# Performance work log

Measured on AMD Instinct MI355X. Metric: run time of the kernel, lower is better.

The kernel has to match this reference:

```python
import jax, jax.numpy as jnp
import numpy as np

B, S, D, H, F = 64, 256, 512, 8, 2048
NB = 2
L = NB + 2 * NB  # blocks_1 (NB) + blocks_2 (2*NB) = 6 attention layers
DH = D // H
FC1, FC2 = 512, 256  # final_fc_dim, final_fc_dim // 2


def setup_inputs() -> dict:
    key = jax.random.key(0)
    ks = jax.random.split(key, 32)
    w = lambda k, shape, s: jax.random.normal(k, shape, dtype=jnp.float32) * s
    sD = D ** -0.5
    return {
        "q_embed_data": w(ks[0], (B, S, D), 1.0),
        "qa_embed_data": w(ks[1], (B, S, D), 1.0),
        "Wq": w(ks[2], (L, D, D), sD), "bq": jnp.zeros((L, D), jnp.float32),
        "Wk": w(ks[3], (L, D, D), sD), "bk": jnp.zeros((L, D), jnp.float32),
        "Wv": w(ks[4], (L, D, D), sD), "bv": jnp.zeros((L, D), jnp.float32),
        "Wo": w(ks[5], (L, D, D), sD), "bo": jnp.zeros((L, D), jnp.float32),
        "gammas": w(ks[6], (L, H), 1.0),
        "ln1_g": jnp.ones((L, D), jnp.float32), "ln1_b": jnp.zeros((L, D), jnp.float32),
        "W1": w(ks[7], (L, D, F), sD), "b1": jnp.zeros((L, F), jnp.float32),
        "W2": w(ks[8], (L, F, D), F ** -0.5), "b2": jnp.zeros((L, D), jnp.float32),
        "ln2_g": jnp.ones((L, D), jnp.float32), "ln2_b": jnp.zeros((L, D), jnp.float32),
        "O1": w(ks[9], (2 * D, FC1), (2 * D) ** -0.5), "bO1": jnp.zeros((FC1,), jnp.float32),
        "O2": w(ks[10], (FC1, FC2), FC1 ** -0.5), "bO2": jnp.zeros((FC2,), jnp.float32),
        "O3": w(ks[11], (FC2, 1), FC2 ** -0.5), "bO3": jnp.zeros((1,), jnp.float32),
    }


def _layer_norm(x, g, b):
    mu = x.mean(-1, keepdims=True)
    var = ((x - mu) ** 2).mean(-1, keepdims=True)
    return (x - mu) * jax.lax.rsqrt(var + 1e-5) * g + b


def _akt_attention(q, k, v, mask, gamma, zero_pad):
    # q,k,v: [B,H,S,DH]; mask: [S,S] bool; gamma: [H]
    neg = jnp.float32(-1e32)
    scores = jnp.einsum('bhqd,bhkd->bhqk', q, k) / np.sqrt(DH).astype(np.float32)
    # monotonic distance-decay (detached in the original): softmax'd scores -> cumulative distance
    sm = jax.nn.softmax(jnp.where(mask, scores, neg), axis=-1) * mask
    sm = jax.lax.stop_gradient(sm)
    distcum = jnp.cumsum(sm, axis=-1)
    disttot = jnp.sum(sm, axis=-1, keepdims=True)
    idx = jnp.arange(S)
    pos = jnp.abs(idx[:, None] - idx[None, :]).astype(jnp.float32)  # |x1 - x2|
    dist = jnp.sqrt(jnp.clip((disttot - distcum) * pos, 0.0, None))
    g = -jax.nn.softplus(gamma)[None, :, None, None]
    total_effect = jnp.clip(jnp.exp(dist * g), 1e-5, 1e5)
    scores = jnp.where(mask, scores * total_effect, neg)
    attn = jax.nn.softmax(scores, axis=-1)
    if zero_pad:
        attn = attn.at[:, :, 0, :].set(0.0)  # zero first query row
    out = jnp.einsum('bhqk,bhkd->bhqd', attn, v)
    return out, attn


def reference(q_embed_data, qa_embed_data, Wq, bq, Wk, bk, Wv, bv, Wo, bo, gammas,
              ln1_g, ln1_b, W1, b1, W2, b2, ln2_g, ln2_b, O1, bO1, O2, bO2, O3, bO3):
    idx = jnp.arange(S)
    mask_incl = idx[:, None] >= idx[None, :]  # mask==1: current + past
    mask_excl = idx[:, None] > idx[None, :]   # mask==0: strictly past

    def block(i, query, key_, vals, incl, zero_pad, apply_pos):
        proj = lambda x, W, b: (x @ W + b).reshape(B, S, H, DH).transpose(0, 2, 1, 3)
        qh, kh, vh = proj(query, Wq[i], bq[i]), proj(key_, Wk[i], bk[i]), proj(vals, Wv[i], bv[i])
        o, attn = _akt_attention(qh, kh, vh, mask_incl if incl else mask_excl, gammas[i], zero_pad)
        o = o.transpose(0, 2, 1, 3).reshape(B, S, D) @ Wo[i] + bo[i]
        q2 = _layer_norm(query + o, ln1_g[i], ln1_b[i])
        if apply_pos:
            h = jax.nn.relu(q2 @ W1[i] + b1[i]) @ W2[i] + b2[i]
            q2 = _layer_norm(q2 + h, ln2_g[i], ln2_b[i])
        return q2, attn

    y = qa_embed_data
    x = q_embed_data
    li = 0
    for _ in range(NB):  # blocks_1: knowledge encoder, self-attn, mask=1
        y, _ = block(li, y, y, y, incl=True, zero_pad=False, apply_pos=True)
        li += 1
    attn = None
    flag_first = True
    for _ in range(2 * NB):  # blocks_2: alternating question self-attn / knowledge retriever
        if flag_first:
            x, _ = block(li, x, x, x, incl=True, zero_pad=False, apply_pos=False)
            flag_first = False
        else:
            x, attn = block(li, x, x, y, incl=False, zero_pad=True, apply_pos=True)
            flag_first = True
        li += 1

    concat_q = jnp.concatenate([x, q_embed_data], axis=-1)  # [B,S,2D]
    h = jax.nn.relu(concat_q @ O1 + bO1)
    h = jax.nn.relu(h @ O2 + bO2)
    preds = jax.nn.sigmoid((h @ O3 + bO3)[..., 0])  # [B,S]
    return preds
```

## Files before the change

kernel.cpp:

```cpp
#include <hip/hip_runtime.h>

typedef unsigned short u16;
typedef unsigned int u32;
typedef short short8 __attribute__((ext_vector_type(8)));
typedef float f32x4 __attribute__((ext_vector_type(4)));

#define DEV static __device__ __forceinline__

DEV u16 f2bf(float f) {
  u32 u = __builtin_bit_cast(u32, f);
  u32 r = u + 0x7FFFu + ((u >> 16) & 1u);
  return (u16)(r >> 16);
}
DEV float bf2f(u16 h) { u32 u = ((u32)h) << 16; return __builtin_bit_cast(float, u); }

DEV u32 cvtpk(float lo, float hi_) {
  u32 r;
  asm("v_cvt_pk_bf16_f32 %0, %1, %2" : "=v"(r) : "v"(lo), "v"(hi_));
  return r;
}

DEV void async16(const u16* g, u16* l) {
  __builtin_amdgcn_global_load_lds((const __attribute__((address_space(1))) void*)g,
                                   (__attribute__((address_space(3))) void*)l, 16, 0, 0);
}

template<bool RELU, bool OUTBF, bool RESID, bool SPLIT3>
__global__ __launch_bounds__(256, 2) void gemm_kernel(
    const u16* __restrict__ A, const u16* __restrict__ A2, int KA,
    int lda, int lda2,
    const u16* __restrict__ Bt, int K,
    const float* __restrict__ bias, const float* __restrict__ resid,
    float* __restrict__ Cf, u16* __restrict__ Cb, u16* __restrict__ Cb2, u16* __restrict__ Cb3,
    int ldc)
{
  __shared__ u16 smem[2][16384];
  const int tid = threadIdx.x, wave = tid >> 6, lane = tid & 63;
  const int m0 = blockIdx.x * 128, n0 = blockIdx.y * 128;
  const int wr = wave >> 1, wc = wave & 1;
  const int lj = lane & 15, hi = lane >> 4;

  f32x4 acc[4][4];
  const f32x4 zz = {0.f, 0.f, 0.f, 0.f};
#pragma unroll
  for (int i = 0; i < 4; i++)
#pragma unroll
    for (int j = 0; j < 4; j++) acc[i][j] = zz;

  const int nkt = K / 64;

  auto stage = [&](int buf, int kt) {
    int kofs = kt * 64;
    const u16* sa; int la;
    if (kofs < KA) { sa = A + kofs; la = lda; }
    else           { sa = A2 + (kofs - KA); la = lda2; }
#pragma unroll
    for (int i = 0; i < 8; i++) {
      int c = wave * 8 + i;
      if (c < 16) {
        const u16* g = sa + (size_t)(m0 + c * 8 + (lane >> 3)) * la + (lane & 7) * 8;
        async16(g, &smem[buf][c * 512]);
      } else {
        const u16* g = Bt + (size_t)(n0 + (c - 16) * 8 + (lane >> 3)) * K + kofs + (lane & 7) * 8;
        async16(g, &smem[buf][c * 512]);
      }
    }
  };

  stage(0, 0);
  int cur = 0;
  for (int kt = 0; kt < nkt; kt++) {
    __syncthreads();
    if (kt + 1 < nkt) stage(cur ^ 1, kt + 1);
    const u16* la_ = &smem[cur][0];
    const u16* lb_ = &smem[cur][8192];
#pragma unroll
    for (int ks = 0; ks < 2; ks++) {
      short8 af[4], bfr[4];
#pragma unroll
      for (int mi = 0; mi < 4; mi++)
        af[mi] = *(const short8*)(la_ + (wr * 64 + mi * 16 + lj) * 64 + ks * 32 + hi * 8);
#pragma unroll
      for (int ni = 0; ni < 4; ni++)
        bfr[ni] = *(const short8*)(lb_ + (wc * 64 + ni * 16 + lj) * 64 + ks * 32 + hi * 8);
#pragma unroll
      for (int mi = 0; mi < 4; mi++)
#pragma unroll
        for (int ni = 0; ni < 4; ni++)
          acc[mi][ni] = __builtin_amdgcn_mfma_f32_16x16x32_bf16(af[mi], bfr[ni], acc[mi][ni], 0, 0, 0);
    }
    cur ^= 1;
  }

  u16* outB = Cb;
  int nloc = n0;
  if (SPLIT3) {
    int sec = n0 >> 9;
    outB = (sec == 0) ? Cb : (sec == 1) ? Cb2 : Cb3;
    nloc = n0 & 511;
  }

  float bv[4];
#pragma unroll
  for (int ni = 0; ni < 4; ni++) bv[ni] = bias[n0 + wc * 64 + ni * 16 + lj];
#pragma unroll
  for (int mi = 0; mi < 4; mi++)
#pragma unroll
    for (int r = 0; r < 4; r++) {
      int row = m0 + wr * 64 + mi * 16 + hi * 4 + r;
      size_t rb = (size_t)row * ldc;
#pragma unroll
      for (int ni = 0; ni < 4; ni++) {
        int col = nloc + wc * 64 + ni * 16 + lj;
        float v = acc[mi][ni][r] + bv[ni];
        if (RESID) v += resid[rb + col];
        if (RELU) v = fmaxf(v, 0.f);
        if (OUTBF) outB[rb + col] = f2bf(v);
        else Cf[rb + col] = v;
      }
    }
}

template<bool INCL, bool ZP>
__global__ __launch_bounds__(512) void attn_kernel(
    const u16* __restrict__ qb, const u16* __restrict__ kb, const u16* __restrict__ vb,
    u16* __restrict__ ob, const float* __restrict__ gammas, int li)
{
  __shared__ u16 smem[32768];
  const int tid = threadIdx.x, wave = tid >> 6, lane = tid & 63;
  const int h = blockIdx.x, b = blockIdx.y;
  const int lj = lane & 15, hi = lane >> 4;
  const size_t rowbase = (size_t)b * 256 * 512 + h * 64;

#pragma unroll
  for (int p = 0; p < 2; p++) {
    int r2 = p * 128 + (tid >> 3) * 2;
    int cc = (tid & 7) * 8;
    union { uint4 v; u16 e[8]; } v0, v1;
    uint4 k0 = *(const uint4*)(kb + rowbase + (size_t)r2 * 512 + cc);
    uint4 k1 = *(const uint4*)(kb + rowbase + (size_t)(r2 + 1) * 512 + cc);
    v0.v = *(const uint4*)(vb + rowbase + (size_t)r2 * 512 + cc);
    v1.v = *(const uint4*)(vb + rowbase + (size_t)(r2 + 1) * 512 + cc);
    *(uint4*)((char*)smem + r2 * 128 + ((cc * 2) ^ ((r2 & 7) << 4))) = k0;
    *(uint4*)((char*)smem + (r2 + 1) * 128 + ((cc * 2) ^ (((r2 + 1) & 7) << 4))) = k1;
#pragma unroll
    for (int i = 0; i < 8; i++) {
      int d = cc + i;
      u32 pk = (u32)v0.e[i] | ((u32)v1.e[i] << 16);
      *(u32*)((char*)smem + 32768 + d * 512 + ((2 * r2) ^ ((d & 7) << 4))) = pk;
    }
  }

  const int qbase = wave * 32;
  const int nrf = 2 * wave + 2;
  const int nsp = wave + 1;

  short8 qfa[2][2];
#pragma unroll
  for (int cf = 0; cf < 2; cf++)
#pragma unroll
    for (int s = 0; s < 2; s++)
      qfa[cf][s] = *(const short8*)(qb + rowbase + (size_t)(qbase + cf * 16 + lj) * 512 + s * 32 + hi * 8);

  float gm = gammas[li * 8 + h];
  float geff = -(gm > 20.f ? gm : log1pf(__expf(gm)));

  __syncthreads();

  const f32x4 zz = {0.f, 0.f, 0.f, 0.f};
  const int hsel = hi >> 1;
  const int sbase = lj + 32 * (hi & 1);

#pragma unroll
  for (int cf = 0; cf < 2; cf++) {
    const int q = qbase + cf * 16 + lj;

    f32x4 acc[16];
#pragma unroll
    for (int rf = 0; rf < 16; rf++) acc[rf] = zz;

#pragma unroll
    for (int rf = 0; rf < 16; rf++) {
      if (rf >= nrf) continue;
      int row = rf * 16 + lj;
#pragma unroll
      for (int s = 0; s < 2; s++) {
        short8 kf = *(const short8*)((char*)smem + row * 128 + ((s * 64 + hi * 16) ^ ((row & 7) << 4)));
        acc[rf] = __builtin_amdgcn_mfma_f32_16x16x32_bf16(kf, qfa[cf][s], acc[rf], 0, 0, 0);
      }
    }

    float mx = -1e30f;
#pragma unroll
    for (int rf = 0; rf < 16; rf++) {
      if (rf >= nrf) continue;
#pragma unroll
      for (int r = 0; r < 4; r++) {
        acc[rf][r] *= 0.125f;
        int k = rf * 16 + hi * 4 + r;
        bool valid = INCL ? (k <= q) : (k < q);
        mx = fmaxf(mx, valid ? acc[rf][r] : -1e30f);
      }
    }
    mx = fmaxf(mx, __shfl_xor(mx, 16));
    mx = fmaxf(mx, __shfl_xor(mx, 32));
    float sum = 0.f;
#pragma unroll
    for (int rf = 0; rf < 16; rf++) {
      if (rf >= nrf) continue;
#pragma unroll
      for (int r = 0; r < 4; r++) {
        int k = rf * 16 + hi * 4 + r;
        bool valid = INCL ? (k <= q) : (k < q);
        sum += valid ? __expf(acc[rf][r] - mx) : 0.f;
      }
    }
    sum += __shfl_xor(sum, 16);
    sum += __shfl_xor(sum, 32);
    float m1 = mx;
    float inv1 = sum > 0.f ? 1.f / sum : 0.f;
    float dtot = sum > 0.f ? 1.f : 0.f;

    float run = 0.f;
#pragma unroll
    for (int rf = 0; rf < 16; rf++) {
      if (rf >= nrf) continue;
      float p[4];
      float pa = 0.f;
#pragma unroll
      for (int r = 0; r < 4; r++) {
        int k = rf * 16 + hi * 4 + r;
        bool valid = INCL ? (k <= q) : (k < q);
        float smv = valid ? __expf(acc[rf][r] - m1) * inv1 : 0.f;
        pa += smv;
        p[r] = pa;
      }
      float t = p[3];
      float v = t;
      float u1 = __shfl_up(v, 16); v += (hi >= 1) ? u1 : 0.f;
      float u2 = __shfl_up(v, 32); v += (hi >= 2) ? u2 : 0.f;
      float T = __shfl(v, lj + 48);
      float cbase = run + (v - t);
#pragma unroll
      for (int r = 0; r < 4; r++) {
        int k = rf * 16 + hi * 4 + r;
        bool valid = INCL ? (k <= q) : (k < q);
        float tail = fmaxf(dtot - (cbase + p[r]), 0.f);
        float pos = (float)(q - k);
        float dist = sqrtf(tail * pos);
        float te = fmaxf(__expf(dist * geff), 1e-5f);
        acc[rf][r] = valid ? acc[rf][r] * te : -1e32f;
      }
      run += T;
    }

    float mx2 = -3.0e38f;
#pragma unroll
    for (int rf = 0; rf < 16; rf++) {
      if (rf >= nrf) continue;
#pragma unroll
      for (int r = 0; r < 4; r++) mx2 = fmaxf(mx2, acc[rf][r]);
    }
    mx2 = fmaxf(mx2, __shfl_xor(mx2, 16));
    mx2 = fmaxf(mx2, __shfl_xor(mx2, 32));
    float sum2 = 0.f;
#pragma unroll
    for (int rf = 0; rf < 16; rf++) {
      if (rf >= nrf) continue;
#pragma unroll
      for (int r = 0; r < 4; r++) {
        float ev = __expf(acc[rf][r] - mx2);
        acc[rf][r] = ev;
        sum2 += ev;
      }
    }
    sum2 += __shfl_xor(sum2, 16);
    sum2 += __shfl_xor(sum2, 32);
    float inv = 1.f / sum2;
    if (ZP) { if (q == 0) inv = 0.f; }
#pragma unroll
    for (int rf = 0; rf < 16; rf++) {
      if (rf >= nrf) continue;
#pragma unroll
      for (int r = 0; r < 4; r++) acc[rf][r] *= inv;
    }

    f32x4 oacc[4];
#pragma unroll
    for (int j = 0; j < 4; j++) oacc[j] = zz;

#pragma unroll
    for (int sp = 0; sp < 8; sp++) {
      if (sp >= nsp) continue;
      u32 a0 = cvtpk(acc[2 * sp][0],     acc[2 * sp][1]);
      u32 a1 = cvtpk(acc[2 * sp][2],     acc[2 * sp][3]);
      u32 b0 = cvtpk(acc[2 * sp + 1][0], acc[2 * sp + 1][1]);
      u32 b1 = cvtpk(acc[2 * sp + 1][2], acc[2 * sp + 1][3]);
      u32 pw[4];
#pragma unroll
      for (int t = 0; t < 4; t++) {
        int src = sbase + 16 * (t >> 1);
        u32 za = (u32)__shfl((int)((t & 1) ? a1 : a0), src);
        u32 zb = (u32)__shfl((int)((t & 1) ? b1 : b0), src);
        pw[t] = hsel ? zb : za;
      }
      short8 pf = __builtin_bit_cast(short8, *(uint4*)pw);
#pragma unroll
      for (int nf = 0; nf < 4; nf++) {
        int d = nf * 16 + lj;
        short8 vf = *(const short8*)((char*)smem + 32768 + d * 512 + ((sp * 64 + hi * 16) ^ ((d & 7) << 4)));
        oacc[nf] = __builtin_amdgcn_mfma_f32_16x16x32_bf16(pf, vf, oacc[nf], 0, 0, 0);
      }
    }

#pragma unroll
    for (int r = 0; r < 4; r++) {
      int qr = qbase + cf * 16 + hi * 4 + r;
      size_t obase = (size_t)(b * 256 + qr) * 512 + h * 64;
#pragma unroll
      for (int nf = 0; nf < 4; nf++)
        ob[obase + nf * 16 + lj] = f2bf(oacc[nf][r]);
    }
  }
}

__global__ __launch_bounds__(256) void ln_kernel(const float* __restrict__ x,
    const float* __restrict__ g, const float* __restrict__ bt,
    float* __restrict__ outF, u16* __restrict__ outB)
{
  int row = blockIdx.x * 4 + (threadIdx.x >> 6), lane = threadIdx.x & 63;
  const float* xr = x + (size_t)row * 512 + lane * 8;
  float4 a = *(const float4*)xr;
  float4 c = *(const float4*)(xr + 4);
  float s = a.x + a.y + a.z + a.w + c.x + c.y + c.z + c.w;
  float q = a.x*a.x + a.y*a.y + a.z*a.z + a.w*a.w + c.x*c.x + c.y*c.y + c.z*c.z + c.w*c.w;
#pragma unroll
  for (int m = 1; m <= 32; m <<= 1) { s += __shfl_xor(s, m); q += __shfl_xor(q, m); }
  float mu = s * (1.f / 512.f);
  float var = q * (1.f / 512.f) - mu * mu;
  float rs = rsqrtf(fmaxf(var, 0.f) + 1e-5f);
  const float* gr = g + lane * 8; const float* br = bt + lane * 8;
  float4 g0 = *(const float4*)gr, g1v = *(const float4*)(gr + 4);
  float4 b0 = *(const float4*)br, b1v = *(const float4*)(br + 4);
  float y[8];
  y[0]=(a.x-mu)*rs*g0.x+b0.x; y[1]=(a.y-mu)*rs*g0.y+b0.y; y[2]=(a.z-mu)*rs*g0.z+b0.z; y[3]=(a.w-mu)*rs*g0.w+b0.w;
  y[4]=(c.x-mu)*rs*g1v.x+b1v.x; y[5]=(c.y-mu)*rs*g1v.y+b1v.y; y[6]=(c.z-mu)*rs*g1v.z+b1v.z; y[7]=(c.w-mu)*rs*g1v.w+b1v.w;
  float* of = outF + (size_t)row * 512 + lane * 8;
  *(float4*)of = make_float4(y[0], y[1], y[2], y[3]);
  *(float4*)(of + 4) = make_float4(y[4], y[5], y[6], y[7]);
  union { uint4 v; u16 e[8]; } pk;
#pragma unroll
  for (int i = 0; i < 8; i++) pk.e[i] = f2bf(y[i]);
  *(uint4*)(outB + (size_t)row * 512 + lane * 8) = pk.v;
}

__global__ void cvt_kernel(const float* __restrict__ in, u16* __restrict__ out, int n8)
{
  int i = blockIdx.x * 256 + threadIdx.x;
  if (i >= n8) return;
  float4 a = ((const float4*)in)[2 * i], c = ((const float4*)in)[2 * i + 1];
  union { uint4 v; u16 e[8]; } pk;
  pk.e[0]=f2bf(a.x); pk.e[1]=f2bf(a.y); pk.e[2]=f2bf(a.z); pk.e[3]=f2bf(a.w);
  pk.e[4]=f2bf(c.x); pk.e[5]=f2bf(c.y); pk.e[6]=f2bf(c.z); pk.e[7]=f2bf(c.w);
  ((uint4*)out)[i] = pk.v;
}

__global__ void trans_kernel(const float* __restrict__ in, u16* __restrict__ out,
                             int R, int C, size_t istr, size_t ostr)
{
  __shared__ float tile[32][33];
  in += (size_t)blockIdx.z * istr;
  out += (size_t)blockIdx.z * ostr;
  int c0 = blockIdx.x * 32, r0 = blockIdx.y * 32;
  int tx = threadIdx.x & 31, ty = threadIdx.x >> 5;
#pragma unroll
  for (int i = 0; i < 4; i++) tile[ty + i * 8][tx] = in[(size_t)(r0 + ty + i * 8) * C + c0 + tx];
  __syncthreads();
#pragma unroll
  for (int i = 0; i < 4; i++) out[(size_t)(c0 + ty + i * 8) * R + r0 + tx] = f2bf(tile[tx][ty + i * 8]);
}

__global__ void bias_concat_kernel(const float* __restrict__ bq, const float* __restrict__ bk,
                                   const float* __restrict__ bv, float* __restrict__ out)
{
  int t = blockIdx.x * 256 + threadIdx.x;
  if (t >= 6 * 1536) return;
  int li = t / 1536, c = t % 1536;
  float v = (c < 512) ? bq[li * 512 + c]
          : (c < 1024) ? bk[li * 512 + c - 512]
                       : bv[li * 512 + c - 1024];
  out[t] = v;
}

__global__ __launch_bounds__(256) void pred_kernel(const u16* __restrict__ h2,
    const float* __restrict__ O3, const float* __restrict__ bO3, float* __restrict__ out)
{
  int row = blockIdx.x * 4 + (threadIdx.x >> 6), lane = threadIdx.x & 63;
  union { uint2 v; u16 e[4]; } hv;
  hv.v = *(const uint2*)(h2 + (size_t)row * 256 + lane * 4);
  float d = 0.f;
#pragma unroll
  for (int i = 0; i < 4; i++) d += bf2f(hv.e[i]) * O3[lane * 4 + i];
#pragma unroll
  for (int m = 1; m <= 32; m <<= 1) d += __shfl_xor(d, m);
  if (lane == 0) out[row] = 1.f / (1.f + expf(-(d + bO3[0])));
}

extern "C" void kernel_launch(void* const* d_in, const int* in_sizes, int n_in,
                              void* d_out, int out_size, void* d_ws, size_t ws_size,
                              hipStream_t stream)
{
  const float* qe   = (const float*)d_in[0];
  const float* qa   = (const float*)d_in[1];
  const float* Wq   = (const float*)d_in[2];  const float* bq  = (const float*)d_in[3];
  const float* Wk   = (const float*)d_in[4];  const float* bk  = (const float*)d_in[5];
  const float* Wv   = (const float*)d_in[6];  const float* bv  = (const float*)d_in[7];
  const float* Wo   = (const float*)d_in[8];  const float* bo  = (const float*)d_in[9];
  const float* gam  = (const float*)d_in[10];
  const float* ln1g = (const float*)d_in[11]; const float* ln1b = (const float*)d_in[12];
  const float* W1   = (const float*)d_in[13]; const float* b1  = (const float*)d_in[14];
  const float* W2   = (const float*)d_in[15]; const float* b2  = (const float*)d_in[16];
  const float* ln2g = (const float*)d_in[17]; const float* ln2b = (const float*)d_in[18];
  const float* O1   = (const float*)d_in[19]; const float* bO1 = (const float*)d_in[20];
  const float* O2   = (const float*)d_in[21]; const float* bO2 = (const float*)d_in[22];
  const float* O3   = (const float*)d_in[23]; const float* bO3 = (const float*)d_in[24];
  float* preds = (float*)d_out;

  const int M = 16384;
  const int BIG = 0x3fffffff;
  char* ws = (char*)d_ws;
  size_t off = 0;
  auto alloc = [&](size_t bytes) { char* p = ws + off; off += (bytes + 255) & ~(size_t)255; return p; };

  u16* wqkvt = (u16*)alloc((size_t)6*1536*512*2);
  u16* wot   = (u16*)alloc((size_t)6*512*512*2);
  u16* w1t   = (u16*)alloc((size_t)6*2048*512*2);
  u16* w2t   = (u16*)alloc((size_t)6*512*2048*2);
  u16* o1t   = (u16*)alloc((size_t)512*1024*2);
  u16* o2t   = (u16*)alloc((size_t)256*512*2);
  float* bqkv = (float*)alloc((size_t)6*1536*4);
  u16* qx  = (u16*)alloc((size_t)M*512*2);
  u16* sA  = (u16*)alloc((size_t)M*512*2);
  u16* sB  = (u16*)alloc((size_t)M*512*2);
  float* g1 = (float*)alloc((size_t)M*512*4);
  u16* region = (u16*)alloc((size_t)M*2048*2);
  u16* qbf = region;
  u16* kbf = region + (size_t)M*512;
  u16* vbf = region + (size_t)2*M*512;
  u16* obf = region + (size_t)3*M*512;
  u16* h1  = region;
  u16* hd1 = region;
  u16* hd2 = region + (size_t)2*M*512;
  (void)ws_size; (void)in_sizes; (void)n_in; (void)out_size;

  trans_kernel<<<dim3(16, 16, 6), 256, 0, stream>>>(Wq, wqkvt,                          512, 512,  (size_t)512*512,  (size_t)1536*512);
  trans_kernel<<<dim3(16, 16, 6), 256, 0, stream>>>(Wk, wqkvt + (size_t)512*512,        512, 512,  (size_t)512*512,  (size_t)1536*512);
  trans_kernel<<<dim3(16, 16, 6), 256, 0, stream>>>(Wv, wqkvt + (size_t)1024*512,       512, 512,  (size_t)512*512,  (size_t)1536*512);
  trans_kernel<<<dim3(16, 16, 6), 256, 0, stream>>>(Wo, wot,                            512, 512,  (size_t)512*512,  (size_t)512*512);
  trans_kernel<<<dim3(64, 16, 6), 256, 0, stream>>>(W1, w1t,                            512, 2048, (size_t)512*2048, (size_t)2048*512);
  trans_kernel<<<dim3(16, 64, 6), 256, 0, stream>>>(W2, w2t,                            2048, 512, (size_t)2048*512, (size_t)512*2048);
  trans_kernel<<<dim3(16, 32, 1), 256, 0, stream>>>(O1, o1t,                            1024, 512, 0, 0);
  trans_kernel<<<dim3(8, 16, 1),  256, 0, stream>>>(O2, o2t,                            512, 256,  0, 0);
  bias_concat_kernel<<<36, 256, 0, stream>>>(bq, bk, bv, bqkv);
  cvt_kernel<<<4096, 256, 0, stream>>>(qe, qx, M * 512 / 8);
  cvt_kernel<<<4096, 256, 0, stream>>>(qa, sA, M * 512 / 8);

  const u16* curB = sA;
  const float* curF = qa;
  const u16* yfin = nullptr;
  const dim3 gP(128, 4), gF1(128, 16), gA(8, 64);

  for (int li = 0; li < 6; li++) {
    bool ffn  = (li == 0 || li == 1 || li == 3 || li == 5);
    bool excl = (li == 3 || li == 5);
    size_t wqkv_off = (size_t)li * 1536 * 512;

    if (!excl) {
      gemm_kernel<false, true, false, true><<<dim3(128, 12), 256, 0, stream>>>(
          curB, curB, BIG, 512, 512, wqkvt + wqkv_off, 512, bqkv + li * 1536,
          nullptr, nullptr, qbf, kbf, vbf, 512);
    } else {
      gemm_kernel<false, true, false, true><<<dim3(128, 8), 256, 0, stream>>>(
          curB, curB, BIG, 512, 512, wqkvt + wqkv_off, 512, bqkv + li * 1536,
          nullptr, nullptr, qbf, kbf, nullptr, 512);
      gemm_kernel<false, true, false, false><<<dim3(128, 4), 256, 0, stream>>>(
          yfin, yfin, BIG, 512, 512, wqkvt + wqkv_off + (size_t)1024 * 512, 512, bv + li * 512,
          nullptr, nullptr, vbf, nullptr, nullptr, 512);
    }

    if (!excl) attn_kernel<true,  false><<<gA, 512, 0, stream>>>(qbf, kbf, vbf, obf, gam, li);
    else       attn_kernel<false, true ><<<gA, 512, 0, stream>>>(qbf, kbf, vbf, obf, gam, li);

    gemm_kernel<false, false, true, false><<<gP, 256, 0, stream>>>(
        obf, obf, BIG, 512, 512, wot + (size_t)li * 512 * 512, 512, bo + li * 512,
        curF, g1, nullptr, nullptr, nullptr, 512);

    ln_kernel<<<4096, 256, 0, stream>>>(g1, ln1g + li * 512, ln1b + li * 512, g1, sB);
    curB = sB; curF = g1;

    if (ffn) {
      gemm_kernel<true, true, false, false><<<gF1, 256, 0, stream>>>(
          curB, curB, BIG, 512, 512, w1t + (size_t)li * 2048 * 512, 512, b1 + li * 2048,
          nullptr, nullptr, h1, nullptr, nullptr, 2048);
      gemm_kernel<false, false, true, false><<<gP, 256, 0, stream>>>(
          h1, h1, BIG, 2048, 2048, w2t + (size_t)li * 512 * 2048, 2048, b2 + li * 512,
          g1, g1, nullptr, nullptr, nullptr, 512);
      u16* nB = (li < 2) ? sA : sB;
      ln_kernel<<<4096, 256, 0, stream>>>(g1, ln2g + li * 512, ln2b + li * 512, g1, nB);
      curB = nB;
    }
    if (li == 1) { yfin = curB; curB = qx; curF = qe; }
  }

  gemm_kernel<true, true, false, false><<<dim3(128, 4), 256, 0, stream>>>(
      curB, qx, 512, 512, 512, o1t, 1024, bO1, nullptr, nullptr, hd1, nullptr, nullptr, 512);
  gemm_kernel<true, true, false, false><<<dim3(128, 2), 256, 0, stream>>>(
      hd1, hd1, BIG, 512, 512, o2t, 512, bO2, nullptr, nullptr, hd2, nullptr, nullptr, 256);
  pred_kernel<<<4096, 256, 0, stream>>>(hd2, O3, bO3, preds);
}
```

Measured before the change: 1.490 ms.

## Balance causal attention work across waves and cache softmax exponentials

Each wave now takes query tiles t and 15-t instead of two adjacent tiles, so every wave does about the same amount of causal work and the slowest wave is no longer the one holding the last rows. The exponentials from the first softmax pass are kept in a register array and reused for the cumulative-distance pass instead of being recomputed. The per-tile loop bounds now depend on the tile index, which makes the unrolled guards less uniform. The extra 16-entry array adds register pressure and may lower occupancy or cause spills.

```diff
diff --git a/kernel.cpp b/kernel.cpp
--- a/kernel.cpp
+++ b/kernel.cpp
@@ -151,16 +151,16 @@
     }
   }
 
-  const int qbase = wave * 32;
-  const int nrf = 2 * wave + 2;
-  const int nsp = wave + 1;
+  const int qt0 = wave, qt1 = 15 - wave;
 
   short8 qfa[2][2];
 #pragma unroll
-  for (int cf = 0; cf < 2; cf++)
+  for (int cf = 0; cf < 2; cf++) {
+    int t = cf ? qt1 : qt0;
 #pragma unroll
     for (int s = 0; s < 2; s++)
-      qfa[cf][s] = *(const short8*)(qb + rowbase + (size_t)(qbase + cf * 16 + lj) * 512 + s * 32 + hi * 8);
+      qfa[cf][s] = *(const short8*)(qb + rowbase + (size_t)(t * 16 + lj) * 512 + s * 32 + hi * 8);
+  }
 
   float gm = gammas[li * 8 + h];
   float geff = -(gm > 20.f ? gm : log1pf(__expf(gm)));
@@ -173,9 +173,13 @@
 
 #pragma unroll
   for (int cf = 0; cf < 2; cf++) {
-    const int q = qbase + cf * 16 + lj;
-
-    f32x4 acc[16];
+    const int t = cf ? qt1 : qt0;
+    const int qb0 = t * 16;
+    const int q = qb0 + lj;
+    const int nrf = t + 1;
+    const int nsp = (t + 2) >> 1;
+
+    f32x4 acc[16], E[16];
 #pragma unroll
     for (int rf = 0; rf < 16; rf++) acc[rf] = zz;
 
@@ -212,12 +216,13 @@
       for (int r = 0; r < 4; r++) {
         int k = rf * 16 + hi * 4 + r;
         bool valid = INCL ? (k <= q) : (k < q);
-        sum += valid ? __expf(acc[rf][r] - mx) : 0.f;
+        float ev = valid ? __expf(acc[rf][r] - mx) : 0.f;
+        E[rf][r] = ev;
+        sum += ev;
       }
     }
     sum += __shfl_xor(sum, 16);
     sum += __shfl_xor(sum, 32);
-    float m1 = mx;
     float inv1 = sum > 0.f ? 1.f / sum : 0.f;
     float dtot = sum > 0.f ? 1.f : 0.f;
 
@@ -229,18 +234,15 @@
       float pa = 0.f;
 #pragma unroll
       for (int r = 0; r < 4; r++) {
-        int k = rf * 16 + hi * 4 + r;
-        bool valid = INCL ? (k <= q) : (k < q);
-        float smv = valid ? __expf(acc[rf][r] - m1) * inv1 : 0.f;
-        pa += smv;
+        pa += E[rf][r] * inv1;
         p[r] = pa;
       }
-      float t = p[3];
-      float v = t;
+      float tl = p[3];
+      float v = tl;
       float u1 = __shfl_up(v, 16); v += (hi >= 1) ? u1 : 0.f;
       float u2 = __shfl_up(v, 32); v += (hi >= 2) ? u2 : 0.f;
       float T = __shfl(v, lj + 48);
-      float cbase = run + (v - t);
+      float cbase = run + (v - tl);
 #pragma unroll
       for (int r = 0; r < 4; r++) {
         int k = rf * 16 + hi * 4 + r;
@@ -298,11 +300,11 @@
       u32 b1 = cvtpk(acc[2 * sp + 1][2], acc[2 * sp + 1][3]);
       u32 pw[4];
 #pragma unroll
-      for (int t = 0; t < 4; t++) {
-        int src = sbase + 16 * (t >> 1);
-        u32 za = (u32)__shfl((int)((t & 1) ? a1 : a0), src);
-        u32 zb = (u32)__shfl((int)((t & 1) ? b1 : b0), src);
-        pw[t] = hsel ? zb : za;
+      for (int tt = 0; tt < 4; tt++) {
+        int src = sbase + 16 * (tt >> 1);
+        u32 za = (u32)__shfl((int)((tt & 1) ? a1 : a0), src);
+        u32 zb = (u32)__shfl((int)((tt & 1) ? b1 : b0), src);
+        pw[tt] = hsel ? zb : za;
       }
       short8 pf = __builtin_bit_cast(short8, *(uint4*)pw);
 #pragma unroll
@@ -315,7 +317,7 @@
 
 #pragma unroll
     for (int r = 0; r < 4; r++) {
-      int qr = qbase + cf * 16 + hi * 4 + r;
+      int qr = qb0 + hi * 4 + r;
       size_t obase = (size_t)(b * 256 + qr) * 512 + h * 64;
 #pragma unroll
       for (int nf = 0; nf < 4; nf++)
```

Result: faster. 1.385 ms (-7.1%).
